# Kernel tuning notes

Hardware: AMD Instinct MI355X
Metric: run time of the kernel (lower is better)

Reference implementation:

```python
import jax, jax.numpy as jnp
import numpy as np

T, B, IN, H, L = 2048, 64, 512, 512, 2


def _uniform(key, shape, lo, hi):
    return jax.random.uniform(key, shape, jnp.float32, lo, hi)


def setup_inputs() -> dict:
    key = jax.random.key(0)
    ks = jax.random.split(key, 16)
    initrange = 0.1
    inp = {
        "x": jax.random.normal(ks[0], (T, B, IN), jnp.float32),
        "h0": jnp.zeros((L, B, H), jnp.float32),
        "c0": jnp.zeros((L, B, H), jnp.float32),
        # layer 0: input_size -> H, layer 1: H -> H
        "Wx0": _uniform(ks[1], (4 * H, IN), -initrange, initrange),
        "Wh0": _uniform(ks[2], (4 * H, H), -initrange, initrange),
        "bx0": _uniform(ks[3], (4 * H,), -0.04, 0.04),
        "bh0": _uniform(ks[4], (4 * H,), -0.04, 0.04),
        "Wx1": _uniform(ks[5], (4 * H, H), -initrange, initrange),
        "Wh1": _uniform(ks[6], (4 * H, H), -initrange, initrange),
        "bx1": _uniform(ks[7], (4 * H,), -0.04, 0.04),
        "bh1": _uniform(ks[8], (4 * H,), -0.04, 0.04),
    }
    return inp


def _lstm_layer(x_seq, h0, c0, Wx, Wh, bx, bh):
    """Run one LSTM layer over the full sequence with lax.scan.
    x_seq: [T, B, D_in]; h0, c0: [B, H]. Gate order (i, f, c_ex, o)."""
    def step(carry, xt):
        h, c = carry
        gates = xt @ Wx.T + bx + h @ Wh.T + bh  # [B, 4H]
        i, f, g, o = jnp.split(gates, 4, axis=-1)
        c = jax.nn.sigmoid(f) * c + jax.nn.sigmoid(i) * jnp.tanh(g)
        h = jax.nn.sigmoid(o) * jnp.tanh(c)
        return (h, c), h

    (hT, cT), ys = jax.lax.scan(step, (h0, c0), x_seq)
    return ys, hT, cT


def reference(x, h0, c0, Wx0, Wh0, bx0, bh0, Wx1, Wh1, bx1, bh1):
    params = [(Wx0, Wh0, bx0, bh0), (Wx1, Wh1, bx1, bh1)]
    out = x
    h_fin, c_fin = [], []
    for layer in range(L):
        Wx, Wh, bx, bh = params[layer]
        out, hT, cT = _lstm_layer(out, h0[layer], c0[layer], Wx, Wh, bx, bh)
        h_fin.append(hT)
        c_fin.append(cT)
    # dropout factor is 0.0 -> identity between layers
    return out, (jnp.stack(h_fin, 0), jnp.stack(c_fin, 0))
```

## Files before the change

### kernel.cpp

```cpp
#include <hip/hip_runtime.h>
#include <hip/hip_bf16.h>
#include <cstdint>
#include <cstddef>

#define T_STEPS 2048
#define BATCH   64
#define HID     512
#define BH      (BATCH * HID)
#define NBLK    256
#define TPB     256
#define NBLK_L  128
#define RING    16

typedef float        f32x4 __attribute__((ext_vector_type(4)));
typedef short        s16x8 __attribute__((ext_vector_type(8)));
typedef int          i32x4 __attribute__((ext_vector_type(4)));
typedef unsigned int u32x2 __attribute__((ext_vector_type(2)));

#define HB1_OFF   0x000000u
#define FLAGS_OFF 0x020000u
#define HS_OFF    0x230000u
#define XB_OFF    0x400000u

static __device__ __forceinline__ short f2bf(float v) {
  __hip_bfloat16 b = __float2bfloat16(v);
  return *reinterpret_cast<short*>(&b);
}
static __device__ __forceinline__ float sigm(float x) {
  return 1.0f / (1.0f + __expf(-x));
}

#define LOADC16(dst, base, off)                                        \
  asm volatile("global_load_dwordx4 %0, %1, off offset:%c2 sc0 sc1"    \
               : "=v"(dst) : "v"(base), "i"(off))
#define STOREC8(base, val)                                             \
  asm volatile("global_store_dwordx2 %0, %1, off sc0 sc1"              \
               :: "v"(base), "v"(val) : "memory")
#define VMDRAIN asm volatile("s_waitcnt vmcnt(0)" ::: "memory")

#define MFMA(acc, af, bf) \
  acc = __builtin_amdgcn_mfma_f32_16x16x32_bf16(af, bf, acc, 0, 0, 0)

static __device__ __forceinline__ void poll4(const int* p) {
  i32x4 v;
  for (;;) {
    asm volatile("global_load_dwordx4 %0, %1, off sc0 sc1\n\t"
                 "s_waitcnt vmcnt(0)"
                 : "=v"(v) : "v"(p) : "memory");
    if ((v[0] & v[1] & v[2] & v[3]) != 0) return;
    __builtin_amdgcn_s_sleep(1);
  }
}

__global__ void prep_h(const float* __restrict__ h0, short* __restrict__ hs,
                       short* __restrict__ hb1) {
  int idx = blockIdx.x * blockDim.x + threadIdx.x;
  if (idx >= 2 * BH) return;
  short v = f2bf(h0[idx]);
  if (idx < BH) hs[idx] = v;
  else hb1[idx - BH] = v;
}

__global__ void prep_xb(const float* __restrict__ x, short* __restrict__ xb) {
  size_t i = ((size_t)blockIdx.x * blockDim.x + threadIdx.x) * 8;
  if (i >= (size_t)T_STEPS * BH) return;
  f32x4 v0 = *reinterpret_cast<const f32x4*>(x + i);
  f32x4 v1 = *reinterpret_cast<const f32x4*>(x + i + 4);
  s16x8 o;
  o[0] = f2bf(v0[0]); o[1] = f2bf(v0[1]); o[2] = f2bf(v0[2]); o[3] = f2bf(v0[3]);
  o[4] = f2bf(v1[0]); o[5] = f2bf(v1[1]); o[6] = f2bf(v1[2]); o[7] = f2bf(v1[3]);
  *reinterpret_cast<s16x8*>(xb + i) = o;
}

struct KArgs {
  const short* xb;
  const float* c0;
  const float *Wx0, *Wh0, *bx0, *bh0;
  const float *Wx1, *Wh1, *bx1, *bh1;
  short* hs;
  short* hb1;
  int* flags;
  float *yout, *hfin, *cfin;
};

template <int LAY>
static __device__ __forceinline__ void run_layer(const KArgs& a, int bidL,
                                                 int tid) {
  const int nt = tid >> 6;
  const int l = tid & 63, lane15 = l & 15, jloc = l >> 4, koff = jloc * 8;
  const int row0 = bidL * 16;
  const int b = nt * 16 + lane15;
  const int kbase = row0 >> 2;
  const int kcol = kbase + jloc;

  const float* WxL = LAY ? a.Wx1 : a.Wx0;
  const float* WhL = LAY ? a.Wh1 : a.Wh0;
  const float* bxL = LAY ? a.bx1 : a.bx0;
  const float* bhL = LAY ? a.bh1 : a.bh0;

  const int r = row0 + lane15;
  const int srow = (r & 3) * HID + (r >> 2);
  s16x8 wreg[32];
#pragma unroll
  for (int ks = 0; ks < 32; ++ks) {
    const float* src = (ks < 16)
        ? (WxL + (size_t)srow * 512 + ks * 32 + koff)
        : (WhL + (size_t)srow * 512 + (ks - 16) * 32 + koff);
    f32x4 v0 = *reinterpret_cast<const f32x4*>(src);
    f32x4 v1 = *reinterpret_cast<const f32x4*>(src + 4);
    s16x8 wv;
    wv[0] = f2bf(v0[0]); wv[1] = f2bf(v0[1]); wv[2] = f2bf(v0[2]); wv[3] = f2bf(v0[3]);
    wv[4] = f2bf(v1[0]); wv[5] = f2bf(v1[1]); wv[6] = f2bf(v1[2]); wv[7] = f2bf(v1[3]);
    wreg[ks] = wv;
  }
  const float bI = bxL[kcol]           + bhL[kcol];
  const float bF = bxL[HID + kcol]     + bhL[HID + kcol];
  const float bG = bxL[2 * HID + kcol] + bhL[2 * HID + kcol];
  const float bO = bxL[3 * HID + kcol] + bhL[3 * HID + kcol];
  float c = a.c0[LAY * BH + b * HID + kcol];

  int* f0 = a.flags;
  int* f1 = a.flags + (size_t)T_STEPS * NBLK_L;

  for (int t = 0; t < T_STEPS; ++t) {
    if (LAY == 0) {
      if (t > 0 && tid < 32) poll4(f0 + (size_t)(t - 1) * NBLK_L + tid * 4);
      if (t >= RING && tid >= 32 && tid < 64)
        poll4(f1 + (size_t)(t - RING) * NBLK_L + (tid - 32) * 4);
    } else {
      if (tid < 32) poll4(f0 + (size_t)t * NBLK_L + tid * 4);
      else if (t > 0 && tid < 64)
        poll4(f1 + (size_t)(t - 1) * NBLK_L + (tid - 32) * 4);
    }
    __syncthreads();

    f32x4 acc0 = {0.f, 0.f, 0.f, 0.f}, acc1 = {0.f, 0.f, 0.f, 0.f};
    s16x8 frag[16];

    if (LAY == 0) {
      const short* xp = a.xb + ((size_t)t * BATCH + b) * HID + koff;
#pragma unroll
      for (int i = 0; i < 16; ++i)
        frag[i] = *reinterpret_cast<const s16x8*>(xp + i * 32);
    } else {
      const short* xp = a.hs + (size_t)((t + 1) & (RING - 1)) * BH
                        + b * HID + koff;
#pragma unroll
      for (int i = 0; i < 16; ++i) LOADC16(frag[i], xp, i * 64);
      VMDRAIN;
      __builtin_amdgcn_sched_barrier(0);
    }
#pragma unroll
    for (int ks = 0; ks < 16; ++ks) {
      if (ks & 1) { MFMA(acc1, wreg[ks], frag[ks]); } else { MFMA(acc0, wreg[ks], frag[ks]); }
    }

    const short* hp = (LAY ? a.hb1 + (t & 1) * BH
                           : a.hs + (size_t)(t & (RING - 1)) * BH)
                      + b * HID + koff;
#pragma unroll
    for (int i = 0; i < 16; ++i) LOADC16(frag[i], hp, i * 64);
    VMDRAIN;
    __builtin_amdgcn_sched_barrier(0);
#pragma unroll
    for (int ks = 16; ks < 32; ++ks) {
      if (ks & 1) { MFMA(acc1, wreg[ks], frag[ks - 16]); } else { MFMA(acc0, wreg[ks], frag[ks - 16]); }
    }

    float gi = acc0[0] + acc1[0] + bI;
    float gf = acc0[1] + acc1[1] + bF;
    float gg = acc0[2] + acc1[2] + bG;
    float go = acc0[3] + acc1[3] + bO;
    float iv = sigm(gi), fv = sigm(gf);
    float gv = tanhf(gg), ov = sigm(go);
    c = fv * c + iv * gv;
    float hv = ov * tanhf(c);

    int hvi = (int)(unsigned short)f2bf(hv);
    int h1 = __shfl(hvi, lane15 + 16);
    int h2 = __shfl(hvi, lane15 + 32);
    int h3 = __shfl(hvi, lane15 + 48);
    short* dsth = (LAY ? a.hb1 + ((t + 1) & 1) * BH
                       : a.hs + (size_t)((t + 1) & (RING - 1)) * BH)
                  + b * HID + kbase;
    if (jloc == 0) {
      u32x2 pk;
      pk[0] = (unsigned)(hvi & 0xffff) | ((unsigned)h1 << 16);
      pk[1] = (unsigned)(h2 & 0xffff) | ((unsigned)h3 << 16);
      STOREC8(dsth, pk);
    }
    if (LAY == 1) {
      int y0 = __float_as_int(hv);
      int y1 = __shfl(y0, lane15 + 16);
      int y2 = __shfl(y0, lane15 + 32);
      int y3 = __shfl(y0, lane15 + 48);
      if (jloc == 0) {
        f32x4 yv = {__int_as_float(y0), __int_as_float(y1),
                    __int_as_float(y2), __int_as_float(y3)};
        __builtin_nontemporal_store(
            yv, reinterpret_cast<f32x4*>(a.yout + ((size_t)t * BATCH + b) * HID + kbase));
      }
    }
    if (t == T_STEPS - 1) {
      a.hfin[LAY * BH + b * HID + kcol] = hv;
      a.cfin[LAY * BH + b * HID + kcol] = c;
    }

    VMDRAIN;
    __syncthreads();
    if (tid == 0) {
      int one = 1;
      int* fp = (LAY ? f1 : f0) + (size_t)t * NBLK_L + bidL;
      asm volatile("global_store_dword %0, %1, off sc0 sc1"
                   :: "v"(fp), "v"(one) : "memory");
    }
  }
}

__global__ __launch_bounds__(TPB, 2) void lstm_fused(KArgs a) {
  const int bid = blockIdx.x;
  if (bid < NBLK_L) run_layer<0>(a, bid, threadIdx.x);
  else              run_layer<1>(a, bid - NBLK_L, threadIdx.x);
}

extern "C" void kernel_launch(void* const* d_in, const int* in_sizes, int n_in,
                              void* d_out, int out_size, void* d_ws, size_t ws_size,
                              hipStream_t stream) {
  const float* x   = (const float*)d_in[0];
  const float* h0  = (const float*)d_in[1];
  const float* c0  = (const float*)d_in[2];
  const float* Wx0 = (const float*)d_in[3];
  const float* Wh0 = (const float*)d_in[4];
  const float* bx0 = (const float*)d_in[5];
  const float* bh0 = (const float*)d_in[6];
  const float* Wx1 = (const float*)d_in[7];
  const float* Wh1 = (const float*)d_in[8];
  const float* bx1 = (const float*)d_in[9];
  const float* bh1 = (const float*)d_in[10];

  char* ws = (char*)d_ws;
  short* hb1  = (short*)(ws + HB1_OFF);
  int* flags  = (int*)(ws + FLAGS_OFF);
  short* hs   = (short*)(ws + HS_OFF);
  short* xb   = (short*)(ws + XB_OFF);

  float* yout = (float*)d_out;
  float* hfin = yout + (size_t)T_STEPS * BH;
  float* cfin = hfin + 2 * BH;

  hipMemsetAsync(flags, 0, (size_t)2 * T_STEPS * NBLK_L * sizeof(int), stream);
  prep_xb<<<(int)(((size_t)T_STEPS * BH / 8 + 255) / 256), 256, 0, stream>>>(x, xb);
  prep_h<<<(2 * BH + 255) / 256, 256, 0, stream>>>(h0, hs, hb1);

  KArgs ka{xb, c0, Wx0, Wh0, bx0, bh0, Wx1, Wh1, bx1, bh1,
           hs, hb1, flags, yout, hfin, cfin};
  void* params[] = {&ka};
  hipLaunchCooperativeKernel((void*)lstm_fused, dim3(NBLK), dim3(TPB), params, 0,
                             stream);
}
```

Baseline: 16.83 ms.

## Stage Wx in LDS, overlap x/h loads, deepen ring, publish via atomics

Moves the input-weight fragments from registers into shared memory so only the recurrent weights stay in registers, freeing VGPRs. Issues the x-input and h-state loads together and waits partially (vmcnt 16), so the input MFMAs run while the recurrent loads are in flight. Grows the layer-0 to layer-1 ring buffer from 16 to 64 steps to loosen coupling between the two layers. Publishes h values and flags with atomic swaps instead of coherent stores, which changes the cross-block synchronisation path. It also adds per-step LDS reads and a larger workspace footprint.

```diff
diff --git a/kernel.cpp b/kernel.cpp
--- a/kernel.cpp
+++ b/kernel.cpp
@@ -10,7 +10,7 @@
 #define NBLK    256
 #define TPB     256
 #define NBLK_L  128
-#define RING    16
+#define RING    64
 
 typedef float        f32x4 __attribute__((ext_vector_type(4)));
 typedef short        s16x8 __attribute__((ext_vector_type(8)));
@@ -20,7 +20,7 @@
 #define HB1_OFF   0x000000u
 #define FLAGS_OFF 0x020000u
 #define HS_OFF    0x230000u
-#define XB_OFF    0x400000u
+#define XB_OFF    0x640000u
 
 static __device__ __forceinline__ short f2bf(float v) {
   __hip_bfloat16 b = __float2bfloat16(v);
@@ -33,10 +33,14 @@
 #define LOADC16(dst, base, off)                                        \
   asm volatile("global_load_dwordx4 %0, %1, off offset:%c2 sc0 sc1"    \
                : "=v"(dst) : "v"(base), "i"(off))
-#define STOREC8(base, val)                                             \
-  asm volatile("global_store_dwordx2 %0, %1, off sc0 sc1"              \
+#define LOADP16(dst, base, off)                                        \
+  asm volatile("global_load_dwordx4 %0, %1, off offset:%c2"            \
+               : "=v"(dst) : "v"(base), "i"(off))
+#define ATOMPUB8(base, val)                                            \
+  asm volatile("global_atomic_swap_x2 %0, %1, off sc1"                 \
                :: "v"(base), "v"(val) : "memory")
-#define VMDRAIN asm volatile("s_waitcnt vmcnt(0)" ::: "memory")
+#define VMDRAIN  asm volatile("s_waitcnt vmcnt(0)" ::: "memory")
+#define VMWAIT16 asm volatile("s_waitcnt vmcnt(16)" ::: "memory")
 
 #define MFMA(acc, af, bf) \
   acc = __builtin_amdgcn_mfma_f32_16x16x32_bf16(af, bf, acc, 0, 0, 0)
@@ -85,7 +89,7 @@
 
 template <int LAY>
 static __device__ __forceinline__ void run_layer(const KArgs& a, int bidL,
-                                                 int tid) {
+                                                 int tid, short (*wl)[520]) {
   const int nt = tid >> 6;
   const int l = tid & 63, lane15 = l & 15, jloc = l >> 4, koff = jloc * 8;
   const int row0 = bidL * 16;
@@ -98,20 +102,34 @@
   const float* bxL = LAY ? a.bx1 : a.bx0;
   const float* bhL = LAY ? a.bh1 : a.bh0;
 
+  {
+    const int rloc = tid >> 4;
+    const int col0 = (tid & 15) * 32;
+    const int rr = row0 + rloc;
+    const int sr = (rr & 3) * HID + (rr >> 2);
+    const float* wsrc = WxL + (size_t)sr * 512 + col0;
+#pragma unroll
+    for (int i = 0; i < 4; ++i) {
+      f32x4 v0 = *reinterpret_cast<const f32x4*>(wsrc + i * 8);
+      f32x4 v1 = *reinterpret_cast<const f32x4*>(wsrc + i * 8 + 4);
+      s16x8 wv;
+      wv[0] = f2bf(v0[0]); wv[1] = f2bf(v0[1]); wv[2] = f2bf(v0[2]); wv[3] = f2bf(v0[3]);
+      wv[4] = f2bf(v1[0]); wv[5] = f2bf(v1[1]); wv[6] = f2bf(v1[2]); wv[7] = f2bf(v1[3]);
+      *reinterpret_cast<s16x8*>(&wl[rloc][col0 + i * 8]) = wv;
+    }
+  }
   const int r = row0 + lane15;
-  const int srow = (r & 3) * HID + (r >> 2);
-  s16x8 wreg[32];
-#pragma unroll
-  for (int ks = 0; ks < 32; ++ks) {
-    const float* src = (ks < 16)
-        ? (WxL + (size_t)srow * 512 + ks * 32 + koff)
-        : (WhL + (size_t)srow * 512 + (ks - 16) * 32 + koff);
+  const int sr2 = (r & 3) * HID + (r >> 2);
+  s16x8 whreg[16];
+#pragma unroll
+  for (int ks = 0; ks < 16; ++ks) {
+    const float* src = WhL + (size_t)sr2 * 512 + ks * 32 + koff;
     f32x4 v0 = *reinterpret_cast<const f32x4*>(src);
     f32x4 v1 = *reinterpret_cast<const f32x4*>(src + 4);
     s16x8 wv;
     wv[0] = f2bf(v0[0]); wv[1] = f2bf(v0[1]); wv[2] = f2bf(v0[2]); wv[3] = f2bf(v0[3]);
     wv[4] = f2bf(v1[0]); wv[5] = f2bf(v1[1]); wv[6] = f2bf(v1[2]); wv[7] = f2bf(v1[3]);
-    wreg[ks] = wv;
+    whreg[ks] = wv;
   }
   const float bI = bxL[kcol]           + bhL[kcol];
   const float bF = bxL[HID + kcol]     + bhL[HID + kcol];
@@ -121,6 +139,7 @@
 
   int* f0 = a.flags;
   int* f1 = a.flags + (size_t)T_STEPS * NBLK_L;
+  __syncthreads();
 
   for (int t = 0; t < T_STEPS; ++t) {
     if (LAY == 0) {
@@ -135,36 +154,36 @@
     __syncthreads();
 
     f32x4 acc0 = {0.f, 0.f, 0.f, 0.f}, acc1 = {0.f, 0.f, 0.f, 0.f};
-    s16x8 frag[16];
+    s16x8 fragX[16], fragH[16];
 
     if (LAY == 0) {
       const short* xp = a.xb + ((size_t)t * BATCH + b) * HID + koff;
 #pragma unroll
-      for (int i = 0; i < 16; ++i)
-        frag[i] = *reinterpret_cast<const s16x8*>(xp + i * 32);
+      for (int i = 0; i < 16; ++i) LOADP16(fragX[i], xp, i * 64);
     } else {
       const short* xp = a.hs + (size_t)((t + 1) & (RING - 1)) * BH
                         + b * HID + koff;
 #pragma unroll
-      for (int i = 0; i < 16; ++i) LOADC16(frag[i], xp, i * 64);
-      VMDRAIN;
-      __builtin_amdgcn_sched_barrier(0);
-    }
-#pragma unroll
-    for (int ks = 0; ks < 16; ++ks) {
-      if (ks & 1) { MFMA(acc1, wreg[ks], frag[ks]); } else { MFMA(acc0, wreg[ks], frag[ks]); }
-    }
-
+      for (int i = 0; i < 16; ++i) LOADC16(fragX[i], xp, i * 64);
+    }
     const short* hp = (LAY ? a.hb1 + (t & 1) * BH
                            : a.hs + (size_t)(t & (RING - 1)) * BH)
                       + b * HID + koff;
 #pragma unroll
-    for (int i = 0; i < 16; ++i) LOADC16(frag[i], hp, i * 64);
+    for (int i = 0; i < 16; ++i) LOADC16(fragH[i], hp, i * 64);
+
+    VMWAIT16;
+    __builtin_amdgcn_sched_barrier(0);
+#pragma unroll
+    for (int ks = 0; ks < 16; ++ks) {
+      s16x8 axf = *reinterpret_cast<const s16x8*>(&wl[lane15][ks * 32 + koff]);
+      if (ks & 1) { MFMA(acc1, axf, fragX[ks]); } else { MFMA(acc0, axf, fragX[ks]); }
+    }
     VMDRAIN;
     __builtin_amdgcn_sched_barrier(0);
 #pragma unroll
-    for (int ks = 16; ks < 32; ++ks) {
-      if (ks & 1) { MFMA(acc1, wreg[ks], frag[ks - 16]); } else { MFMA(acc0, wreg[ks], frag[ks - 16]); }
+    for (int ks = 0; ks < 16; ++ks) {
+      if (ks & 1) { MFMA(acc1, whreg[ks], fragH[ks]); } else { MFMA(acc0, whreg[ks], fragH[ks]); }
     }
 
     float gi = acc0[0] + acc1[0] + bI;
@@ -187,7 +206,7 @@
       u32x2 pk;
       pk[0] = (unsigned)(hvi & 0xffff) | ((unsigned)h1 << 16);
       pk[1] = (unsigned)(h2 & 0xffff) | ((unsigned)h3 << 16);
-      STOREC8(dsth, pk);
+      ATOMPUB8(dsth, pk);
     }
     if (LAY == 1) {
       int y0 = __float_as_int(hv);
@@ -211,16 +230,17 @@
     if (tid == 0) {
       int one = 1;
       int* fp = (LAY ? f1 : f0) + (size_t)t * NBLK_L + bidL;
-      asm volatile("global_store_dword %0, %1, off sc0 sc1"
+      asm volatile("global_atomic_swap %0, %1, off sc1"
                    :: "v"(fp), "v"(one) : "memory");
     }
   }
 }
 
 __global__ __launch_bounds__(TPB, 2) void lstm_fused(KArgs a) {
+  __shared__ short wl[16][520];
   const int bid = blockIdx.x;
-  if (bid < NBLK_L) run_layer<0>(a, bid, threadIdx.x);
-  else              run_layer<1>(a, bid - NBLK_L, threadIdx.x);
+  if (bid < NBLK_L) run_layer<0>(a, bid, threadIdx.x, wl);
+  else              run_layer<1>(a, bid - NBLK_L, threadIdx.x, wl);
 }
 
 extern "C" void kernel_launch(void* const* d_in, const int* in_sizes, int n_in,
```

After: 16.50 ms. -2.0%, faster.

## Replace h ring buffer with full history, read fp32 inputs directly, atomic publish

Applied to the files above, without the earlier changes.

Stores layer-0 hidden states for every timestep instead of a 16-slot ring. This removes layer 0's back-pressure poll on layer 1. Layer 1's own recurrent state is now read back as fp32 from the output tensor, and layer 0 reads fp32 x directly, converting in-kernel, so the bf16 x prep pass goes away. The bf16 h loads are issued together with the fp32 loads, and a partial vmcnt wait lets the MFMAs on the bf16 operand start before the fp32 data arrives. Publishes and flags use atomic swaps at device scope instead of sc0 sc1 stores. The cost is about double the per-step operand bytes for the fp32 reads, and plain cached loads must still see data written by other blocks.

```diff
diff --git a/kernel.cpp b/kernel.cpp
--- a/kernel.cpp
+++ b/kernel.cpp
@@ -10,17 +10,15 @@
 #define NBLK    256
 #define TPB     256
 #define NBLK_L  128
-#define RING    16
 
 typedef float        f32x4 __attribute__((ext_vector_type(4)));
 typedef short        s16x8 __attribute__((ext_vector_type(8)));
 typedef int          i32x4 __attribute__((ext_vector_type(4)));
 typedef unsigned int u32x2 __attribute__((ext_vector_type(2)));
 
-#define HB1_OFF   0x000000u
-#define FLAGS_OFF 0x020000u
+#define FLAGS_OFF 0x000000u
+#define H1I_OFF   0x200000u
 #define HS_OFF    0x230000u
-#define XB_OFF    0x400000u
 
 static __device__ __forceinline__ short f2bf(float v) {
   __hip_bfloat16 b = __float2bfloat16(v);
@@ -30,13 +28,17 @@
   return 1.0f / (1.0f + __expf(-x));
 }
 
-#define LOADC16(dst, base, off)                                        \
-  asm volatile("global_load_dwordx4 %0, %1, off offset:%c2 sc0 sc1"    \
+#define LOADP16(dst, base, off)                                        \
+  asm volatile("global_load_dwordx4 %0, %1, off offset:%c2"            \
                : "=v"(dst) : "v"(base), "i"(off))
-#define STOREC8(base, val)                                             \
-  asm volatile("global_store_dwordx2 %0, %1, off sc0 sc1"              \
+#define ATOMPUB8(base, val)                                            \
+  asm volatile("global_atomic_swap_x2 %0, %1, off sc1"                 \
                :: "v"(base), "v"(val) : "memory")
-#define VMDRAIN asm volatile("s_waitcnt vmcnt(0)" ::: "memory")
+#define STOREC16(base, val)                                            \
+  asm volatile("global_store_dwordx4 %0, %1, off sc0 sc1"              \
+               :: "v"(base), "v"(val) : "memory")
+#define VMDRAIN  asm volatile("s_waitcnt vmcnt(0)" ::: "memory")
+#define VMWAIT32 asm volatile("s_waitcnt vmcnt(32)" ::: "memory")
 
 #define MFMA(acc, af, bf) \
   acc = __builtin_amdgcn_mfma_f32_16x16x32_bf16(af, bf, acc, 0, 0, 0)
@@ -53,32 +55,20 @@
 }
 
 __global__ void prep_h(const float* __restrict__ h0, short* __restrict__ hs,
-                       short* __restrict__ hb1) {
+                       float* __restrict__ h1i) {
   int idx = blockIdx.x * blockDim.x + threadIdx.x;
   if (idx >= 2 * BH) return;
-  short v = f2bf(h0[idx]);
-  if (idx < BH) hs[idx] = v;
-  else hb1[idx - BH] = v;
-}
-
-__global__ void prep_xb(const float* __restrict__ x, short* __restrict__ xb) {
-  size_t i = ((size_t)blockIdx.x * blockDim.x + threadIdx.x) * 8;
-  if (i >= (size_t)T_STEPS * BH) return;
-  f32x4 v0 = *reinterpret_cast<const f32x4*>(x + i);
-  f32x4 v1 = *reinterpret_cast<const f32x4*>(x + i + 4);
-  s16x8 o;
-  o[0] = f2bf(v0[0]); o[1] = f2bf(v0[1]); o[2] = f2bf(v0[2]); o[3] = f2bf(v0[3]);
-  o[4] = f2bf(v1[0]); o[5] = f2bf(v1[1]); o[6] = f2bf(v1[2]); o[7] = f2bf(v1[3]);
-  *reinterpret_cast<s16x8*>(xb + i) = o;
+  if (idx < BH) hs[idx] = f2bf(h0[idx]);
+  else h1i[idx - BH] = h0[idx];
 }
 
 struct KArgs {
-  const short* xb;
+  const float* x;
   const float* c0;
   const float *Wx0, *Wh0, *bx0, *bh0;
   const float *Wx1, *Wh1, *bx1, *bh1;
   short* hs;
-  short* hb1;
+  const float* h1i;
   int* flags;
   float *yout, *hfin, *cfin;
 };
@@ -125,8 +115,6 @@
   for (int t = 0; t < T_STEPS; ++t) {
     if (LAY == 0) {
       if (t > 0 && tid < 32) poll4(f0 + (size_t)(t - 1) * NBLK_L + tid * 4);
-      if (t >= RING && tid >= 32 && tid < 64)
-        poll4(f1 + (size_t)(t - RING) * NBLK_L + (tid - 32) * 4);
     } else {
       if (tid < 32) poll4(f0 + (size_t)t * NBLK_L + tid * 4);
       else if (t > 0 && tid < 64)
@@ -135,36 +123,38 @@
     __syncthreads();
 
     f32x4 acc0 = {0.f, 0.f, 0.f, 0.f}, acc1 = {0.f, 0.f, 0.f, 0.f};
-    s16x8 frag[16];
-
-    if (LAY == 0) {
-      const short* xp = a.xb + ((size_t)t * BATCH + b) * HID + koff;
-#pragma unroll
-      for (int i = 0; i < 16; ++i)
-        frag[i] = *reinterpret_cast<const s16x8*>(xp + i * 32);
-    } else {
-      const short* xp = a.hs + (size_t)((t + 1) & (RING - 1)) * BH
-                        + b * HID + koff;
-#pragma unroll
-      for (int i = 0; i < 16; ++i) LOADC16(frag[i], xp, i * 64);
-      VMDRAIN;
-      __builtin_amdgcn_sched_barrier(0);
-    }
+    s16x8 fragB[16];
+    f32x4 s32[32];
+
+    const short* bp = a.hs + (size_t)(LAY ? t + 1 : t) * BH + b * HID + koff;
+#pragma unroll
+    for (int i = 0; i < 16; ++i) LOADP16(fragB[i], bp, i * 64);
+    const float* sp = (LAY ? (t ? a.yout + (size_t)(t - 1) * BH : a.h1i)
+                           : a.x + (size_t)t * BH)
+                      + b * HID + koff;
+#pragma unroll
+    for (int i = 0; i < 16; ++i) {
+      LOADP16(s32[2 * i], sp, i * 128);
+      LOADP16(s32[2 * i + 1], sp, i * 128 + 16);
+    }
+
+    VMWAIT32;
+    __builtin_amdgcn_sched_barrier(0);
 #pragma unroll
     for (int ks = 0; ks < 16; ++ks) {
-      if (ks & 1) { MFMA(acc1, wreg[ks], frag[ks]); } else { MFMA(acc0, wreg[ks], frag[ks]); }
-    }
-
-    const short* hp = (LAY ? a.hb1 + (t & 1) * BH
-                           : a.hs + (size_t)(t & (RING - 1)) * BH)
-                      + b * HID + koff;
-#pragma unroll
-    for (int i = 0; i < 16; ++i) LOADC16(frag[i], hp, i * 64);
+      const s16x8 wf = wreg[LAY ? ks : ks + 16];
+      if (ks & 1) { MFMA(acc1, wf, fragB[ks]); } else { MFMA(acc0, wf, fragB[ks]); }
+    }
     VMDRAIN;
     __builtin_amdgcn_sched_barrier(0);
 #pragma unroll
-    for (int ks = 16; ks < 32; ++ks) {
-      if (ks & 1) { MFMA(acc1, wreg[ks], frag[ks - 16]); } else { MFMA(acc0, wreg[ks], frag[ks - 16]); }
+    for (int ks = 0; ks < 16; ++ks) {
+      f32x4 v0 = s32[2 * ks], v1 = s32[2 * ks + 1];
+      s16x8 bfr;
+      bfr[0] = f2bf(v0[0]); bfr[1] = f2bf(v0[1]); bfr[2] = f2bf(v0[2]); bfr[3] = f2bf(v0[3]);
+      bfr[4] = f2bf(v1[0]); bfr[5] = f2bf(v1[1]); bfr[6] = f2bf(v1[2]); bfr[7] = f2bf(v1[3]);
+      const s16x8 wf = wreg[LAY ? ks + 16 : ks];
+      if (ks & 1) { MFMA(acc1, wf, bfr); } else { MFMA(acc0, wf, bfr); }
     }
 
     float gi = acc0[0] + acc1[0] + bI;
@@ -176,20 +166,19 @@
     c = fv * c + iv * gv;
     float hv = ov * tanhf(c);
 
-    int hvi = (int)(unsigned short)f2bf(hv);
-    int h1 = __shfl(hvi, lane15 + 16);
-    int h2 = __shfl(hvi, lane15 + 32);
-    int h3 = __shfl(hvi, lane15 + 48);
-    short* dsth = (LAY ? a.hb1 + ((t + 1) & 1) * BH
-                       : a.hs + (size_t)((t + 1) & (RING - 1)) * BH)
-                  + b * HID + kbase;
-    if (jloc == 0) {
-      u32x2 pk;
-      pk[0] = (unsigned)(hvi & 0xffff) | ((unsigned)h1 << 16);
-      pk[1] = (unsigned)(h2 & 0xffff) | ((unsigned)h3 << 16);
-      STOREC8(dsth, pk);
-    }
-    if (LAY == 1) {
+    if (LAY == 0) {
+      int hvi = (int)(unsigned short)f2bf(hv);
+      int h1 = __shfl(hvi, lane15 + 16);
+      int h2 = __shfl(hvi, lane15 + 32);
+      int h3 = __shfl(hvi, lane15 + 48);
+      if (jloc == 0) {
+        short* dsth = a.hs + (size_t)(t + 1) * BH + b * HID + kbase;
+        u32x2 pk;
+        pk[0] = (unsigned)(hvi & 0xffff) | ((unsigned)h1 << 16);
+        pk[1] = (unsigned)(h2 & 0xffff) | ((unsigned)h3 << 16);
+        ATOMPUB8(dsth, pk);
+      }
+    } else {
       int y0 = __float_as_int(hv);
       int y1 = __shfl(y0, lane15 + 16);
       int y2 = __shfl(y0, lane15 + 32);
@@ -197,8 +186,7 @@
       if (jloc == 0) {
         f32x4 yv = {__int_as_float(y0), __int_as_float(y1),
                     __int_as_float(y2), __int_as_float(y3)};
-        __builtin_nontemporal_store(
-            yv, reinterpret_cast<f32x4*>(a.yout + ((size_t)t * BATCH + b) * HID + kbase));
+        STOREC16(a.yout + (size_t)t * BH + b * HID + kbase, yv);
       }
     }
     if (t == T_STEPS - 1) {
@@ -211,7 +199,7 @@
     if (tid == 0) {
       int one = 1;
       int* fp = (LAY ? f1 : f0) + (size_t)t * NBLK_L + bidL;
-      asm volatile("global_store_dword %0, %1, off sc0 sc1"
+      asm volatile("global_atomic_swap %0, %1, off sc1"
                    :: "v"(fp), "v"(one) : "memory");
     }
   }
@@ -239,21 +227,19 @@
   const float* bh1 = (const float*)d_in[10];
 
   char* ws = (char*)d_ws;
-  short* hb1  = (short*)(ws + HB1_OFF);
-  int* flags  = (int*)(ws + FLAGS_OFF);
-  short* hs   = (short*)(ws + HS_OFF);
-  short* xb   = (short*)(ws + XB_OFF);
+  int*   flags = (int*)(ws + FLAGS_OFF);
+  float* h1i   = (float*)(ws + H1I_OFF);
+  short* hs    = (short*)(ws + HS_OFF);
 
   float* yout = (float*)d_out;
   float* hfin = yout + (size_t)T_STEPS * BH;
   float* cfin = hfin + 2 * BH;
 
   hipMemsetAsync(flags, 0, (size_t)2 * T_STEPS * NBLK_L * sizeof(int), stream);
-  prep_xb<<<(int)(((size_t)T_STEPS * BH / 8 + 255) / 256), 256, 0, stream>>>(x, xb);
-  prep_h<<<(2 * BH + 255) / 256, 256, 0, stream>>>(h0, hs, hb1);
-
-  KArgs ka{xb, c0, Wx0, Wh0, bx0, bh0, Wx1, Wh1, bx1, bh1,
-           hs, hb1, flags, yout, hfin, cfin};
+  prep_h<<<(2 * BH + 255) / 256, 256, 0, stream>>>(h0, hs, h1i);
+
+  KArgs ka{x, c0, Wx0, Wh0, bx0, bh0, Wx1, Wh1, bx1, bh1,
+           hs, h1i, flags, yout, hfin, cfin};
   void* params[] = {&ka};
   hipLaunchCooperativeKernel((void*)lstm_fused, dim3(NBLK), dim3(TPB), params, 0,
                              stream);
```

After: 25.48 ms. +51.4%, slower.
